# Kernel optimization log

Hardware: AMD Instinct MI355X
Metric: run time of the kernel (lower is better)

## Reference

```python
import jax, jax.numpy as jnp
import numpy as np

B, C, H, W = 512, 3, 64, 32
K = 2                      # fractional pool kernel size
HOUT, WOUT = 38, 16        # floor(64*0.6), floor(32*0.5)
HID = 128                  # RNN hidden size
D = C * HOUT               # RNN input size = 114


def _frac_starts(in_size, out_size, k, u=0.5):
    # PyTorch fractional-max-pool interval formula with deterministic sample u
    alpha = (in_size - k) / (out_size - 1)
    i = np.arange(out_size - 1)
    starts = np.floor((i + u) * alpha) - np.floor(u * alpha)
    return np.concatenate([starts, [in_size - k]]).astype(np.int32)

ROW = _frac_starts(H, HOUT, K)   # (HOUT,) window start rows
COL = _frac_starts(W, WOUT, K)   # (WOUT,) window start cols


def setup_inputs() -> dict:
    key = jax.random.key(0)
    ks = jax.random.split(key, 5)
    s = 1.0 / np.sqrt(HID)  # torch RNNCell init scale
    return {
        "x": jax.random.normal(ks[0], (B, C, H, W), jnp.float32),
        "W_ih": jax.random.uniform(ks[1], (HID, D), jnp.float32, -s, s),
        "W_hh": jax.random.uniform(ks[2], (HID, HID), jnp.float32, -s, s),
        "b_ih": jax.random.uniform(ks[3], (HID,), jnp.float32, -s, s),
        "b_hh": jax.random.uniform(ks[4], (HID,), jnp.float32, -s, s),
    }


def reference(x, W_ih, W_hh, b_ih, b_hh):
    # 1) fractional max pool, kernel 2: pairwise max over gathered window starts
    xr = jnp.maximum(x[:, :, ROW, :], x[:, :, ROW + 1, :])          # (B,C,HOUT,W)
    pooled = jnp.maximum(xr[:, :, :, COL], xr[:, :, :, COL + 1])    # (B,C,HOUT,WOUT)
    # 2) exact (erf-based) GELU, matching torch nn.GELU default
    act = jax.nn.gelu(pooled, approximate=False)
    # 3) sequence over width: (WOUT, B, C*HOUT), C-major flatten matches torch view
    seq = act.transpose(3, 0, 1, 2).reshape(WOUT, B, D)
    # 4) vanilla RNNCell across time via scan
    def step(h, xt):
        h = jnp.tanh(xt @ W_ih.T + b_ih + h @ W_hh.T + b_hh)
        return h, h
    _, outs = jax.lax.scan(step, jnp.zeros((B, HID), x.dtype), seq)  # (WOUT,B,HID)
    # 5) temporal mean + tanh
    t_mean = jnp.tanh(outs.mean(axis=0))                             # (B,HID)
    # 6) modulate by global spatial mean of pooled; torch broadcasting of
    #    (B,HID) * (B,1,1,1) yields (B,1,B,HID) — replicated faithfully
    s_mean = pooled.mean(axis=(1, 2, 3), keepdims=True)              # (B,1,1,1)
    return t_mean * s_mean                                           # (B,1,B,HID)
```

## Files before the change

### kernel.cpp

```cpp
#include <hip/hip_runtime.h>
#include <math.h>

#define BB   512
#define CC   3
#define HH   64
#define WW   32
#define HOUT 38
#define WOUT 16
#define HID  128
#define DD   114
#define SEQP 120
#define WROW 132
#define NPOOL (CC*HOUT*WOUT)

typedef float f32x4 __attribute__((ext_vector_type(4)));

#define WS_SMEAN 0
#define WS_TMEAN 512

__global__ __launch_bounds__(256, 2)
void k1_fused(const float* __restrict__ x,
              const float* __restrict__ Wih,
              const float* __restrict__ Whh,
              const float* __restrict__ bih,
              const float* __restrict__ bhh,
              float* __restrict__ s_mean,
              float* __restrict__ t_mean)
{
    __shared__ __align__(16) float wst[64 * WROW];
    __shared__ __align__(16) float seq[WOUT][SEQP];
    __shared__ __align__(16) float Zl[WOUT][HID];
    __shared__ __align__(16) float hbuf[2][HID];
    __shared__ float psum[HID];
    __shared__ float red[256];
    __shared__ int   rowl[HOUT];

    const int tid  = threadIdx.x;
    const int half = tid >> 7;
    const int k    = tid & 127;
    const int b    = blockIdx.x;

    if (tid < HOUT) {
        double alpha = (double)(HH - 2) / (double)(HOUT - 1);
        rowl[tid] = (tid < HOUT - 1)
            ? (int)(floor((tid + 0.5) * alpha) - floor(0.5 * alpha))
            : (HH - 2);
    }
    if (tid < HID) hbuf[0][tid] = 0.f;
    if (tid < 96)  seq[tid / 6][DD + tid % 6] = 0.f;

    {
        const f32x4* xg = (const f32x4*)(x + (size_t)b * (CC*HH*WW));
        f32x4*       xd = (f32x4*)wst;
        #pragma unroll
        for (int i = 0; i < (CC*HH*WW/4)/256; ++i)
            xd[tid + 256*i] = xg[tid + 256*i];
    }
    __syncthreads();

    float ps = 0.f;
    #pragma unroll
    for (int it = 0; it < 8; ++it) {
        int idx = tid + it*256;
        if (idx < NPOOL) {
            int c  = idx / (HOUT*WOUT);
            int r  = idx % (HOUT*WOUT);
            int ho = r / WOUT;
            int wo = r % WOUT;
            const float* p0 = &wst[c*(HH*WW) + rowl[ho]*WW + 2*wo];
            float m = fmaxf(fmaxf(p0[0], p0[1]), fmaxf(p0[WW], p0[WW+1]));
            ps += m;
            seq[wo][c*HOUT + ho] =
                0.5f * m * (1.f + erff(m * 0.70710678118654752440f));
        }
    }
    red[tid] = ps;
    __syncthreads();
    #pragma unroll
    for (int s = 128; s > 0; s >>= 1) {
        if (tid < s) red[tid] += red[tid + s];
        __syncthreads();
    }
    if (tid == 0) s_mean[b] = red[0] / (float)NPOOL;
    __syncthreads();

    f32x4 wih[15];
    f32x4 whh[16];

    #pragma unroll
    for (int c = 0; c < 2; ++c) {
        const f32x4* g4 = (const f32x4*)(Wih + c*64*DD);
        for (int j4 = tid; j4 < (64*DD)/4; j4 += 256) {
            f32x4 v = g4[j4];
            int j = 4*j4;
            #pragma unroll
            for (int e = 0; e < 4; ++e) {
                int r  = (j + e) / DD;
                int cc = (j + e) - r*DD;
                wst[r*WROW + cc] = v[e];
            }
        }
        for (int j = tid; j < 64*6; j += 256)
            wst[(j/6)*WROW + DD + (j % 6)] = 0.f;
        __syncthreads();
        if ((k >> 6) == c) {
            const f32x4* wr = (const f32x4*)&wst[(k & 63)*WROW + half*60];
            #pragma unroll
            for (int dd = 0; dd < 15; ++dd) wih[dd] = wr[dd];
        }
        __syncthreads();
    }
    #pragma unroll
    for (int c = 0; c < 2; ++c) {
        const f32x4* g4 = (const f32x4*)(Whh + c*64*HID);
        for (int j4 = tid; j4 < (64*HID)/4; j4 += 256) {
            int r  = j4 >> 5;
            int c4 = j4 & 31;
            *(f32x4*)&wst[r*WROW + (c4 << 2)] = g4[j4];
        }
        __syncthreads();
        if ((k >> 6) == c) {
            const f32x4* wr = (const f32x4*)&wst[(k & 63)*WROW + (half << 6)];
            #pragma unroll
            for (int dd = 0; dd < 16; ++dd) whh[dd] = wr[dd];
        }
        __syncthreads();
    }

    float zreg[WOUT];
    #pragma unroll
    for (int t = 0; t < WOUT; ++t) {
        const f32x4* a4 = (const f32x4*)&seq[t][half*60];
        float s0 = 0.f, s1 = 0.f, s2 = 0.f, s3 = 0.f;
        #pragma unroll
        for (int dd = 0; dd < 15; ++dd) {
            f32x4 a = a4[dd];
            s0 = fmaf(wih[dd].x, a.x, s0);
            s1 = fmaf(wih[dd].y, a.y, s1);
            s2 = fmaf(wih[dd].z, a.z, s2);
            s3 = fmaf(wih[dd].w, a.w, s3);
        }
        float zp = (s0 + s1) + (s2 + s3);
        if (half) Zl[t][k] = zp; else zreg[t] = zp;
    }
    __syncthreads();
    const float bias = bih[k] + bhh[k];
    if (!half) {
        #pragma unroll
        for (int t = 0; t < WOUT; ++t) zreg[t] += bias + Zl[t][k];
    }

    float hsum = 0.f;
    #pragma unroll
    for (int t = 0; t < WOUT; ++t) {
        const int cur = t & 1, nxt = cur ^ 1;
        const f32x4* h4 = (const f32x4*)&hbuf[cur][half << 6];
        float s0 = 0.f, s1 = 0.f, s2 = 0.f, s3 = 0.f;
        #pragma unroll
        for (int dd = 0; dd < 16; ++dd) {
            f32x4 hv = h4[dd];
            s0 = fmaf(whh[dd].x, hv.x, s0);
            s1 = fmaf(whh[dd].y, hv.y, s1);
            s2 = fmaf(whh[dd].z, hv.z, s2);
            s3 = fmaf(whh[dd].w, hv.w, s3);
        }
        float up = (s0 + s1) + (s2 + s3);
        if (half) psum[k] = up;
        __syncthreads();
        if (!half) {
            float hn = tanhf(zreg[t] + up + psum[k]);
            hsum += hn;
            hbuf[nxt][k] = hn;
        }
        __syncthreads();
    }
    if (!half) t_mean[b*HID + k] = tanhf(hsum * (1.f / 16.f));
}

__global__ __launch_bounds__(256)
void k2_out(const float* __restrict__ s_mean,
            const float* __restrict__ t_mean,
            f32x4* __restrict__ out)
{
    const int total = BB * BB * HID / 4;
    const f32x4* t4 = (const f32x4*)t_mean;
    const int stride = gridDim.x * blockDim.x;
    for (int g = blockIdx.x * blockDim.x + threadIdx.x; g < total; g += stride) {
        int i = g >> 14;
        int r = g & 16383;
        float s = s_mean[i];
        f32x4 t = t4[r];
        out[g] = s * t;
    }
}

extern "C" void kernel_launch(void* const* d_in, const int* in_sizes, int n_in,
                              void* d_out, int out_size, void* d_ws, size_t ws_size,
                              hipStream_t stream)
{
    const float* x   = (const float*)d_in[0];
    const float* Wih = (const float*)d_in[1];
    const float* Whh = (const float*)d_in[2];
    const float* bih = (const float*)d_in[3];
    const float* bhh = (const float*)d_in[4];

    float* ws     = (float*)d_ws;
    float* s_mean = ws + WS_SMEAN;
    float* t_mean = ws + WS_TMEAN;

    k1_fused<<<dim3(BB), dim3(256), 0, stream>>>(x, Wih, Whh, bih, bhh, s_mean, t_mean);
    k2_out  <<<dim3(4096), dim3(256), 0, stream>>>(s_mean, t_mean, (f32x4*)d_out);
}
```

Baseline: 53.77 us.

## Use wave-shuffle reduction, single-pass W_ih staging, and one-half recurrent matvec

Replaces the shared-memory tree reduction for the spatial mean with a wavefront shuffle reduction plus a four-entry combine. W_ih is now staged into a larger shared buffer in a single pass instead of two halves. The recurrent step has only the first 128 threads compute the full 128-wide dot product with 32 vector registers of W_hh, which removes the partial-sum exchange and one barrier per timestep. The cost is higher register pressure under launch bounds of 2 blocks per SM, a larger shared footprint, and half the threads idle during the serial recurrence.

```diff
diff --git a/kernel.cpp b/kernel.cpp
--- a/kernel.cpp
+++ b/kernel.cpp
@@ -10,7 +10,8 @@
 #define HID  128
 #define DD   114
 #define SEQP 120
-#define WROW 132
+#define WIHP 120
+#define WHHP 132
 #define NPOOL (CC*HOUT*WOUT)
 
 typedef float f32x4 __attribute__((ext_vector_type(4)));
@@ -27,17 +28,18 @@
               float* __restrict__ s_mean,
               float* __restrict__ t_mean)
 {
-    __shared__ __align__(16) float wst[64 * WROW];
+    __shared__ __align__(16) float wst[HID * WIHP];
     __shared__ __align__(16) float seq[WOUT][SEQP];
     __shared__ __align__(16) float Zl[WOUT][HID];
     __shared__ __align__(16) float hbuf[2][HID];
-    __shared__ float psum[HID];
-    __shared__ float red[256];
+    __shared__ float red[4];
     __shared__ int   rowl[HOUT];
 
     const int tid  = threadIdx.x;
     const int half = tid >> 7;
     const int k    = tid & 127;
+    const int wid  = tid >> 6;
+    const int lane = tid & 63;
     const int b    = blockIdx.x;
 
     if (tid < HOUT) {
@@ -74,57 +76,34 @@
                 0.5f * m * (1.f + erff(m * 0.70710678118654752440f));
         }
     }
-    red[tid] = ps;
-    __syncthreads();
-    #pragma unroll
-    for (int s = 128; s > 0; s >>= 1) {
-        if (tid < s) red[tid] += red[tid + s];
-        __syncthreads();
-    }
-    if (tid == 0) s_mean[b] = red[0] / (float)NPOOL;
-    __syncthreads();
-
-    f32x4 wih[15];
-    f32x4 whh[16];
-
-    #pragma unroll
-    for (int c = 0; c < 2; ++c) {
-        const f32x4* g4 = (const f32x4*)(Wih + c*64*DD);
-        for (int j4 = tid; j4 < (64*DD)/4; j4 += 256) {
+    #pragma unroll
+    for (int off = 32; off > 0; off >>= 1) ps += __shfl_down(ps, off);
+    if (lane == 0) red[wid] = ps;
+    __syncthreads();
+    if (tid == 0)
+        s_mean[b] = (red[0] + red[1] + red[2] + red[3]) * (1.f / (float)NPOOL);
+
+    {
+        const f32x4* g4 = (const f32x4*)Wih;
+        for (int j4 = tid; j4 < (HID*DD)/4; j4 += 256) {
             f32x4 v = g4[j4];
-            int j = 4*j4;
+            int j = j4 * 4;
             #pragma unroll
             for (int e = 0; e < 4; ++e) {
                 int r  = (j + e) / DD;
                 int cc = (j + e) - r*DD;
-                wst[r*WROW + cc] = v[e];
+                wst[r*WIHP + cc] = v[e];
             }
         }
-        for (int j = tid; j < 64*6; j += 256)
-            wst[(j/6)*WROW + DD + (j % 6)] = 0.f;
-        __syncthreads();
-        if ((k >> 6) == c) {
-            const f32x4* wr = (const f32x4*)&wst[(k & 63)*WROW + half*60];
-            #pragma unroll
-            for (int dd = 0; dd < 15; ++dd) wih[dd] = wr[dd];
-        }
-        __syncthreads();
-    }
-    #pragma unroll
-    for (int c = 0; c < 2; ++c) {
-        const f32x4* g4 = (const f32x4*)(Whh + c*64*HID);
-        for (int j4 = tid; j4 < (64*HID)/4; j4 += 256) {
-            int r  = j4 >> 5;
-            int c4 = j4 & 31;
-            *(f32x4*)&wst[r*WROW + (c4 << 2)] = g4[j4];
-        }
-        __syncthreads();
-        if ((k >> 6) == c) {
-            const f32x4* wr = (const f32x4*)&wst[(k & 63)*WROW + (half << 6)];
-            #pragma unroll
-            for (int dd = 0; dd < 16; ++dd) whh[dd] = wr[dd];
-        }
-        __syncthreads();
+        for (int j = tid; j < HID*6; j += 256)
+            wst[(j/6)*WIHP + DD + (j % 6)] = 0.f;
+    }
+    __syncthreads();
+    f32x4 wih[15];
+    {
+        const f32x4* wr = (const f32x4*)&wst[k*WIHP + half*60];
+        #pragma unroll
+        for (int dd = 0; dd < 15; ++dd) wih[dd] = wr[dd];
     }
 
     float zreg[WOUT];
@@ -144,33 +123,49 @@
         if (half) Zl[t][k] = zp; else zreg[t] = zp;
     }
     __syncthreads();
-    const float bias = bih[k] + bhh[k];
-    if (!half) {
-        #pragma unroll
-        for (int t = 0; t < WOUT; ++t) zreg[t] += bias + Zl[t][k];
+    {
+        const float bias = bih[k] + bhh[k];
+        if (!half) {
+            #pragma unroll
+            for (int t = 0; t < WOUT; ++t) zreg[t] += bias + Zl[t][k];
+        }
+    }
+
+    f32x4 whh[32];
+    #pragma unroll
+    for (int c = 0; c < 2; ++c) {
+        const f32x4* g4 = (const f32x4*)(Whh + c*64*HID);
+        for (int j4 = tid; j4 < (64*HID)/4; j4 += 256) {
+            int r  = j4 >> 5;
+            int c4 = j4 & 31;
+            *(f32x4*)&wst[r*WHHP + (c4 << 2)] = g4[j4];
+        }
+        __syncthreads();
+        if (!half && (k >> 6) == c) {
+            const f32x4* wr = (const f32x4*)&wst[(k & 63)*WHHP];
+            #pragma unroll
+            for (int dd = 0; dd < 32; ++dd) whh[dd] = wr[dd];
+        }
+        __syncthreads();
     }
 
     float hsum = 0.f;
     #pragma unroll
     for (int t = 0; t < WOUT; ++t) {
-        const int cur = t & 1, nxt = cur ^ 1;
-        const f32x4* h4 = (const f32x4*)&hbuf[cur][half << 6];
-        float s0 = 0.f, s1 = 0.f, s2 = 0.f, s3 = 0.f;
-        #pragma unroll
-        for (int dd = 0; dd < 16; ++dd) {
-            f32x4 hv = h4[dd];
-            s0 = fmaf(whh[dd].x, hv.x, s0);
-            s1 = fmaf(whh[dd].y, hv.y, s1);
-            s2 = fmaf(whh[dd].z, hv.z, s2);
-            s3 = fmaf(whh[dd].w, hv.w, s3);
-        }
-        float up = (s0 + s1) + (s2 + s3);
-        if (half) psum[k] = up;
-        __syncthreads();
         if (!half) {
-            float hn = tanhf(zreg[t] + up + psum[k]);
+            const f32x4* h4 = (const f32x4*)hbuf[t & 1];
+            float s0 = 0.f, s1 = 0.f, s2 = 0.f, s3 = 0.f;
+            #pragma unroll
+            for (int dd = 0; dd < 32; ++dd) {
+                f32x4 hv = h4[dd];
+                s0 = fmaf(whh[dd].x, hv.x, s0);
+                s1 = fmaf(whh[dd].y, hv.y, s1);
+                s2 = fmaf(whh[dd].z, hv.z, s2);
+                s3 = fmaf(whh[dd].w, hv.w, s3);
+            }
+            float hn = tanhf(zreg[t] + ((s0 + s1) + (s2 + s3)));
             hsum += hn;
-            hbuf[nxt][k] = hn;
+            hbuf[(t + 1) & 1][k] = hn;
         }
         __syncthreads();
     }
```

Result: slower. 61.87 us (+15.1%).
